# Kernel optimization log

Hardware: AMD Instinct MI355X
Metric: run time of the kernel (lower is better)

The kernel has to match this reference:

```python
import jax, jax.numpy as jnp
import numpy as np
import math

V, E, H, L, HID, T, B = 32000, 1024, 16, 4, 4096, 1024, 4
HS = E // H  # head size = 64


def _ln(x, g, b, eps=1e-5):
    m = jnp.mean(x, axis=-1, keepdims=True)
    v = jnp.var(x, axis=-1, keepdims=True)
    return (x - m) * jax.lax.rsqrt(v + eps) * g + b


def _pos_encoding(t, e):
    pos = jnp.arange(t, dtype=jnp.float32)[:, None]
    div = jnp.exp(jnp.arange(0, e, 2, dtype=jnp.float32) * (-math.log(10000.0) / e))
    pe = jnp.zeros((t, e), dtype=jnp.float32)
    pe = pe.at[:, 0::2].set(jnp.sin(pos * div))
    pe = pe.at[:, 1::2].set(jnp.cos(pos * div))
    return pe


def setup_inputs() -> dict:
    key = jax.random.key(0)
    ks = jax.random.split(key, 16)
    std = 0.02
    inp = {
        'idx': jax.random.randint(ks[0], (B, T), 0, V),
        'targets': jax.random.randint(ks[1], (B, T), 0, V),
        'tok_emb': jax.random.normal(ks[2], (V, E), jnp.float32) * std,
        'ln1_g': jnp.ones((L, E), jnp.float32),
        'ln1_b': jnp.zeros((L, E), jnp.float32),
        'wq': jax.random.normal(ks[3], (L, H, E, HS), jnp.float32) * std,
        'wk': jax.random.normal(ks[4], (L, H, E, HS), jnp.float32) * std,
        'wv': jax.random.normal(ks[5], (L, H, E, HS), jnp.float32) * std,
        'wo': jax.random.normal(ks[6], (L, H * HS, E), jnp.float32) * std,
        'bo': jnp.zeros((L, E), jnp.float32),
        'ln2_g': jnp.ones((L, E), jnp.float32),
        'ln2_b': jnp.zeros((L, E), jnp.float32),
        'w1': jax.random.normal(ks[7], (L, E, HID), jnp.float32) * std,
        'b1': jnp.zeros((L, HID), jnp.float32),
        'w2': jax.random.normal(ks[8], (L, HID, E), jnp.float32) * std,
        'b2': jnp.zeros((L, E), jnp.float32),
        'lnf_g': jnp.ones((E,), jnp.float32),
        'lnf_b': jnp.zeros((E,), jnp.float32),
        'lm_w': jax.random.normal(ks[9], (E, V), jnp.float32) * std,
        'lm_b': jnp.zeros((V,), jnp.float32),
    }
    return inp


def _forward(idx, targets, tok_emb, ln1_g, ln1_b, wq, wk, wv, wo, bo,
             ln2_g, ln2_b, w1, b1, w2, b2, lnf_g, lnf_b, lm_w, lm_b):
    b, t = idx.shape
    x = tok_emb[idx] * math.sqrt(E)              # [B,T,E], scaled embedding
    x = x + _pos_encoding(t, E)                  # sinusoidal pos enc
    causal = jnp.tril(jnp.ones((t, t), dtype=bool))
    scale = HS ** -0.5
    for l in range(L):
        h = _ln(x, ln1_g[l], ln1_b[l])
        q = jnp.einsum('bte,hek->bhtk', h, wq[l])
        k = jnp.einsum('bte,hek->bhtk', h, wk[l])
        v = jnp.einsum('bte,hek->bhtk', h, wv[l])
        scores = jnp.einsum('bhtk,bhsk->bhts', q, k) * scale
        scores = jnp.where(causal, scores, -jnp.inf)
        w = jax.nn.softmax(scores, axis=-1)
        o = jnp.einsum('bhts,bhsk->bhtk', w, v)
        o = o.transpose(0, 2, 1, 3).reshape(b, t, H * HS)  # concat heads
        x = x + o @ wo[l] + bo[l]
        h2 = _ln(x, ln2_g[l], ln2_b[l])
        x = x + jax.nn.relu(h2 @ w1[l] + b1[l]) @ w2[l] + b2[l]
    x = _ln(x, lnf_g, lnf_b)
    logits = x @ lm_w + lm_b                     # [B,T,V]
    logp = jax.nn.log_softmax(logits, axis=-1)
    loss = -jnp.mean(jnp.take_along_axis(logp, targets[..., None], axis=-1))
    return logits, loss


def reference(idx, targets, tok_emb, ln1_g, ln1_b, wq, wk, wv, wo, bo,
              ln2_g, ln2_b, w1, b1, w2, b2, lnf_g, lnf_b, lm_w, lm_b):
    return _forward(idx, targets, tok_emb, ln1_g, ln1_b, wq, wk, wv, wo, bo,
                    ln2_g, ln2_b, w1, b1, w2, b2, lnf_g, lnf_b, lm_w, lm_b)
```

## Files before the change

### kernel.cpp

```cpp
#include <hip/hip_runtime.h>
#include <hip/hip_bf16.h>
#include <math.h>

#define BB 4
#define TT 1024
#define BT 4096
#define EE 1024
#define HH 16
#define HSZ 64
#define LL 4
#define HID 4096
#define VV 32000
#define LOG2E 1.44269504f

typedef __attribute__((ext_vector_type(8))) __bf16 bf16x8;
typedef __attribute__((ext_vector_type(4))) float f32x4;

#define MFMA16(a, b, c) __builtin_amdgcn_mfma_f32_16x16x32_bf16((a), (b), (c), 0, 0, 0)

__device__ __forceinline__ int swz32(int row, int chunk) {
    return row * 32 + ((chunk ^ ((row >> 1) & 3)) << 3);
}

__device__ __forceinline__ void gload16(const __bf16* g, __bf16* l) {
    __builtin_amdgcn_global_load_lds(
        (const __attribute__((address_space(1))) unsigned int*)g,
        (__attribute__((address_space(3))) unsigned int*)l, 16, 0, 0);
}

__global__ __launch_bounds__(256) void transpose_conv(
    const float* __restrict__ in, __bf16* __restrict__ out,
    int R, int C, long ibs, int bdiv, long os1, long os2)
{
    __shared__ __bf16 tile[64][65];
    const int t = threadIdx.x;
    const int c0 = blockIdx.x * 64, r0 = blockIdx.y * 64;
    const int batch = blockIdx.z;
    const float* ib = in + (size_t)batch * ibs;
    __bf16* ob = out + (size_t)(batch / bdiv) * os1 + (size_t)(batch % bdiv) * os2;
#pragma unroll
    for (int p = 0; p < 4; ++p) {
        const int r = (t >> 4) + p * 16;
        const int c = (t & 15) * 4;
        float4 v = *(const float4*)(ib + (size_t)(r0 + r) * C + c0 + c);
        tile[c + 0][r] = (__bf16)v.x;
        tile[c + 1][r] = (__bf16)v.y;
        tile[c + 2][r] = (__bf16)v.z;
        tile[c + 3][r] = (__bf16)v.w;
    }
    __syncthreads();
#pragma unroll
    for (int p = 0; p < 2; ++p) {
        const int g = t + p * 256;
        const int co = g >> 3, ch = g & 7;
        bf16x8 vv;
#pragma unroll
        for (int j = 0; j < 8; ++j) vv[j] = tile[co][ch * 8 + j];
        *(bf16x8*)(ob + (size_t)(c0 + co) * R + r0 + ch * 8) = vv;
    }
}

__global__ __launch_bounds__(256) void embed_kernel(
    const int* __restrict__ idx, const float* __restrict__ emb, float* __restrict__ x)
{
    const int row = blockIdx.x, tid = threadIdx.x;
    const float pos = (float)(row & (TT - 1));
    const int tok = idx[row];
    const int cb = tid * 4;
    float4 ev = *(const float4*)(emb + (size_t)tok * EE + cb);
    const float kk = -9.2103403720f / (float)EE;
    float pe[4];
#pragma unroll
    for (int j = 0; j < 4; ++j) {
        const int c = cb + j;
        const float div = expf(kk * (float)(c & ~1));
        const float ang = pos * div;
        pe[j] = (c & 1) ? cosf(ang) : sinf(ang);
    }
    float4 r;
    r.x = ev.x * 32.0f + pe[0];
    r.y = ev.y * 32.0f + pe[1];
    r.z = ev.z * 32.0f + pe[2];
    r.w = ev.w * 32.0f + pe[3];
    *(float4*)(x + (size_t)row * EE + cb) = r;
}

__global__ __launch_bounds__(256) void ln_kernel(
    const float* __restrict__ x, const float* __restrict__ g,
    const float* __restrict__ be, __bf16* __restrict__ out)
{
    __shared__ float red[2][4];
    const int row = blockIdx.x, tid = threadIdx.x;
    float4 v = *(const float4*)(x + (size_t)row * EE + tid * 4);
    float s = v.x + v.y + v.z + v.w;
    float ss = v.x * v.x + v.y * v.y + v.z * v.z + v.w * v.w;
#pragma unroll
    for (int m = 1; m < 64; m <<= 1) { s += __shfl_xor(s, m); ss += __shfl_xor(ss, m); }
    if ((tid & 63) == 0) { red[0][tid >> 6] = s; red[1][tid >> 6] = ss; }
    __syncthreads();
    s  = red[0][0] + red[0][1] + red[0][2] + red[0][3];
    ss = red[1][0] + red[1][1] + red[1][2] + red[1][3];
    const float mean = s * (1.0f / EE);
    const float var  = ss * (1.0f / EE) - mean * mean;
    const float rs   = rsqrtf(var + 1e-5f);
    float4 gv = *(const float4*)(g + tid * 4);
    float4 bv = *(const float4*)(be + tid * 4);
    __bf16* o = out + (size_t)row * EE + tid * 4;
    o[0] = (__bf16)((v.x - mean) * rs * gv.x + bv.x);
    o[1] = (__bf16)((v.y - mean) * rs * gv.y + bv.y);
    o[2] = (__bf16)((v.z - mean) * rs * gv.z + bv.z);
    o[3] = (__bf16)((v.w - mean) * rs * gv.w + bv.w);
}

template <int MODE, int GSWZ, int BN>
__global__ __launch_bounds__(256, 2) void gemm_bt(
    const __bf16* __restrict__ A, const __bf16* __restrict__ Bt,
    const float* __restrict__ bias, float* __restrict__ C,
    __bf16* __restrict__ Cb, float2* __restrict__ part,
    int M, int N, int K)
{
    constexpr int JW  = BN / 32;
    constexpr int BSW = BN / 64;
    __shared__ __bf16 As[128 * 32];
    __shared__ __bf16 Bs[BN * 32];
    __shared__ float2 red[(MODE == 4) ? 128 : 1][2];

    const int tid = threadIdx.x;
    const int lane = tid & 63, wid = tid >> 6;
    const int wr = wid >> 1, wc = wid & 1;
    int bm, bn;
    if (GSWZ) {
        const int b = blockIdx.x;
        const int j = b >> 3;
        bm = (b & 7) * 4 + (j & 3);
        bn = j >> 2;
    } else {
        bm = blockIdx.y; bn = blockIdx.x;
    }
    const int m0 = bm * 128, n0 = bn * BN;

    size_t sA[2];  int loA[2];
#pragma unroll
    for (int c = 0; c < 2; ++c) {
        const int seg = wid * 2 + c;
        const int rl = seg * 16 + (lane >> 2);
        const int cl = (lane & 3) ^ ((rl >> 1) & 3);
        loA[c] = seg * 512;
        sA[c] = (size_t)(m0 + rl) * K + cl * 8;
    }
    size_t sB[BSW]; int loB[BSW];
#pragma unroll
    for (int c = 0; c < BSW; ++c) {
        const int seg = wid * BSW + c;
        const int rl = seg * 16 + (lane >> 2);
        const int cl = (lane & 3) ^ ((rl >> 1) & 3);
        loB[c] = seg * 512;
        sB[c] = (size_t)(n0 + rl) * K + cl * 8;
    }

    const int l15 = lane & 15, kch = lane >> 4;
    const int abase = swz32(wr * 64 + l15, kch);
    const int bbase = swz32(wc * (BN / 2) + l15, kch);

    f32x4 acc[4][JW] = {};

    const int nk = K >> 5;
    for (int kt = 0; kt < nk; ++kt) {
        const size_t ko = (size_t)kt * 32;
#pragma unroll
        for (int c = 0; c < 2; ++c)   gload16(A + sA[c] + ko, As + loA[c]);
#pragma unroll
        for (int c = 0; c < BSW; ++c) gload16(Bt + sB[c] + ko, Bs + loB[c]);
        __syncthreads();
        bf16x8 af[4], bfr[JW];
#pragma unroll
        for (int i = 0; i < 4; ++i)  af[i]  = *(const bf16x8*)(As + abase + i * 512);
#pragma unroll
        for (int j = 0; j < JW; ++j) bfr[j] = *(const bf16x8*)(Bs + bbase + j * 512);
#pragma unroll
        for (int i = 0; i < 4; ++i)
#pragma unroll
            for (int j = 0; j < JW; ++j)
                acc[i][j] = MFMA16(af[i], bfr[j], acc[i][j]);
        __syncthreads();
    }

    const int crow = m0 + wr * 64 + ((lane >> 4) << 2);
    const int ccol = n0 + wc * (BN / 2) + l15;
#pragma unroll
    for (int i = 0; i < 4; ++i)
#pragma unroll
        for (int j = 0; j < JW; ++j) {
            const int cc = ccol + j * 16;
#pragma unroll
            for (int r = 0; r < 4; ++r) {
                const size_t oidx = (size_t)(crow + i * 16 + r) * N + cc;
                float v = acc[i][j][r];
                if (MODE == 0) {
                    Cb[oidx] = (__bf16)v;
                } else if (MODE == 1) {
                    v += bias[cc];
                    Cb[oidx] = (__bf16)(v > 0.0f ? v : 0.0f);
                } else if (MODE == 2) {
                    C[oidx] += v + bias[cc];
                } else {
                    __builtin_nontemporal_store(v + bias[cc], &C[oidx]);
                }
            }
        }

    if constexpr (MODE == 4) {
        const int lg = lane >> 4;
#pragma unroll
        for (int i = 0; i < 4; ++i)
#pragma unroll
            for (int r = 0; r < 4; ++r) {
                float tv[4];
                float mx = -1e30f;
#pragma unroll
                for (int j = 0; j < 4; ++j) {
                    tv[j] = acc[i][j][r] + bias[ccol + j * 16];
                    mx = fmaxf(mx, tv[j]);
                }
                mx = fmaxf(mx, __shfl_xor(mx, 1));
                mx = fmaxf(mx, __shfl_xor(mx, 2));
                mx = fmaxf(mx, __shfl_xor(mx, 4));
                mx = fmaxf(mx, __shfl_xor(mx, 8));
                float sm = 0.0f;
#pragma unroll
                for (int j = 0; j < 4; ++j) sm += exp2f((tv[j] - mx) * LOG2E);
                sm += __shfl_xor(sm, 1);
                sm += __shfl_xor(sm, 2);
                sm += __shfl_xor(sm, 4);
                sm += __shfl_xor(sm, 8);
                if (l15 == 0)
                    red[wr * 64 + i * 16 + lg * 4 + r][wc] = make_float2(mx, sm);
            }
        __syncthreads();
        if (tid < 128) {
            const float2 a = red[tid][0], b = red[tid][1];
            const float M2 = fmaxf(a.x, b.x);
            const float S = a.y * exp2f((a.x - M2) * LOG2E)
                          + b.y * exp2f((b.x - M2) * LOG2E);
            part[(size_t)(m0 + tid) * (N >> 7) + bn] = make_float2(M2, S);
        }
    }
}

__global__ __launch_bounds__(64) void attn_kernel(
    const __bf16* __restrict__ qkv, __bf16* __restrict__ out)
{
    __shared__ __bf16 Pl[16 * 32];
    __shared__ __bf16 Vt[64 * 32];
    const int lane = threadIdx.x;
    const int bh = blockIdx.x, b = bh >> 4, hh = bh & 15;
    const int qbase = blockIdx.y * 16;
    const int RS = 3 * EE;
    const __bf16* qp = qkv + (size_t)(b * TT) * RS + hh * HSZ;
    const __bf16* kp = qp + EE;
    const __bf16* vp = qp + 2 * EE;
    const int l15 = lane & 15, lg = lane >> 4;

    bf16x8 aq[2];
#pragma unroll
    for (int e = 0; e < 2; ++e)
        aq[e] = *(const bf16x8*)(qp + (size_t)(qbase + l15) * RS + e * 32 + lg * 8);

    f32x4 ao[4] = {};
    float mrun[4], lrun[4];
#pragma unroll
    for (int r = 0; r < 4; ++r) { mrun[r] = -1e30f; lrun[r] = 0.0f; }

    const int ntile = qbase / 32 + 1;
    for (int st = 0; st < ntile; ++st) {
        const int sbase = st * 32;
        f32x4 as[2] = {};
        __builtin_amdgcn_s_setprio(1);
#pragma unroll
        for (int n = 0; n < 2; ++n)
#pragma unroll
            for (int e = 0; e < 2; ++e) {
                bf16x8 bk = *(const bf16x8*)(kp + (size_t)(sbase + n * 16 + l15) * RS + e * 32 + lg * 8);
                as[n] = MFMA16(aq[e], bk, as[n]);
            }
        __builtin_amdgcn_s_setprio(0);
        {
            const int sl = lane >> 1;
            const int e0 = (lane & 1) * 32;
            const __bf16* vr = vp + (size_t)(sbase + sl) * RS + e0;
#pragma unroll
            for (int c = 0; c < 4; ++c) {
                bf16x8 vvv = *(const bf16x8*)(vr + c * 8);
#pragma unroll
                for (int j = 0; j < 8; ++j)
                    Vt[swz32(e0 + c * 8 + j, sl >> 3) + (sl & 7)] = vvv[j];
            }
        }
#pragma unroll
        for (int r = 0; r < 4; ++r) {
            const int qi = qbase + lg * 4 + r;
            float sc0 = as[0][r] * 0.125f;
            float sc1 = as[1][r] * 0.125f;
            if (sbase + l15 > qi)      sc0 = -1e30f;
            if (sbase + 16 + l15 > qi) sc1 = -1e30f;
            float rm = fmaxf(sc0, sc1);
            rm = fmaxf(rm, __shfl_xor(rm, 1));
            rm = fmaxf(rm, __shfl_xor(rm, 2));
            rm = fmaxf(rm, __shfl_xor(rm, 4));
            rm = fmaxf(rm, __shfl_xor(rm, 8));
            const float mnew = fmaxf(mrun[r], rm);
            const float alpha = exp2f((mrun[r] - mnew) * LOG2E);
            const float p0 = exp2f((sc0 - mnew) * LOG2E);
            const float p1 = exp2f((sc1 - mnew) * LOG2E);
            float rs = p0 + p1;
            rs += __shfl_xor(rs, 1);
            rs += __shfl_xor(rs, 2);
            rs += __shfl_xor(rs, 4);
            rs += __shfl_xor(rs, 8);
            lrun[r] = lrun[r] * alpha + rs;
            mrun[r] = mnew;
#pragma unroll
            for (int n = 0; n < 4; ++n) ao[n][r] *= alpha;
            const int prow = lg * 4 + r;
            Pl[swz32(prow, l15 >> 3) + (l15 & 7)] = (__bf16)p0;
            Pl[swz32(prow, (16 + l15) >> 3) + (l15 & 7)] = (__bf16)p1;
        }
        asm volatile("s_waitcnt lgkmcnt(0)" ::: "memory");
        bf16x8 pa = *(const bf16x8*)(&Pl[swz32(l15, lg)]);
        __builtin_amdgcn_s_setprio(1);
#pragma unroll
        for (int n = 0; n < 4; ++n) {
            bf16x8 bv = *(const bf16x8*)(&Vt[swz32(n * 16 + l15, lg)]);
            ao[n] = MFMA16(pa, bv, ao[n]);
        }
        __builtin_amdgcn_s_setprio(0);
        asm volatile("s_waitcnt lgkmcnt(0)" ::: "memory");
    }
#pragma unroll
    for (int r = 0; r < 4; ++r) {
        const float inv = 1.0f / lrun[r];
        const int row = qbase + lg * 4 + r;
#pragma unroll
        for (int n = 0; n < 4; ++n)
            out[(size_t)(b * TT + row) * EE + hh * HSZ + n * 16 + l15] =
                (__bf16)(ao[n][r] * inv);
    }
}

__global__ __launch_bounds__(256) void loss_reduce(
    const float2* __restrict__ part, const float* __restrict__ logits,
    const int* __restrict__ tgt, float* __restrict__ lossv)
{
    __shared__ float rm[4], rs2[4];
    const int row = blockIdx.x, tid = threadIdx.x;
    float m = -1e30f, s = 0.0f;
    if (tid < (VV >> 7)) {
        const float2 p = part[(size_t)row * (VV >> 7) + tid];
        m = p.x; s = p.y;
    }
#pragma unroll
    for (int k = 1; k < 64; k <<= 1) {
        const float mo = __shfl_xor(m, k), so = __shfl_xor(s, k);
        const float mn = fmaxf(m, mo);
        s = s * exp2f((m - mn) * LOG2E) + so * exp2f((mo - mn) * LOG2E);
        m = mn;
    }
    if ((tid & 63) == 0) { rm[tid >> 6] = m; rs2[tid >> 6] = s; }
    __syncthreads();
    if (tid == 0) {
        float M = rm[0];
#pragma unroll
        for (int w = 1; w < 4; ++w) M = fmaxf(M, rm[w]);
        float S = 0.0f;
#pragma unroll
        for (int w = 0; w < 4; ++w) S += rs2[w] * exp2f((rm[w] - M) * LOG2E);
        lossv[row] = M + logf(S) - logits[(size_t)row * VV + tgt[row]];
    }
}

__global__ __launch_bounds__(256) void loss_final(const float* __restrict__ lossv, float* __restrict__ out)
{
    __shared__ float red[4];
    const int tid = threadIdx.x;
    float s = 0.0f;
    for (int i = tid; i < BT; i += 256) s += lossv[i];
#pragma unroll
    for (int k = 1; k < 64; k <<= 1) s += __shfl_xor(s, k);
    if ((tid & 63) == 0) red[tid >> 6] = s;
    __syncthreads();
    if (tid == 0) out[0] = (red[0] + red[1] + red[2] + red[3]) * (1.0f / BT);
}

extern "C" void kernel_launch(void* const* d_in, const int* in_sizes, int n_in,
                              void* d_out, int out_size, void* d_ws, size_t ws_size,
                              hipStream_t stream)
{
    const int*   idx   = (const int*)d_in[0];
    const int*   tgt   = (const int*)d_in[1];
    const float* temb  = (const float*)d_in[2];
    const float* ln1g  = (const float*)d_in[3];
    const float* ln1b  = (const float*)d_in[4];
    const float* wq    = (const float*)d_in[5];
    const float* wk    = (const float*)d_in[6];
    const float* wv    = (const float*)d_in[7];
    const float* wo    = (const float*)d_in[8];
    const float* bo    = (const float*)d_in[9];
    const float* ln2g  = (const float*)d_in[10];
    const float* ln2b  = (const float*)d_in[11];
    const float* w1    = (const float*)d_in[12];
    const float* b1    = (const float*)d_in[13];
    const float* w2    = (const float*)d_in[14];
    const float* b2    = (const float*)d_in[15];
    const float* lnfg  = (const float*)d_in[16];
    const float* lnfb  = (const float*)d_in[17];
    const float* lm_w  = (const float*)d_in[18];
    const float* lm_b  = (const float*)d_in[19];

    float* logits  = (float*)d_out;
    float* lossout = logits + (size_t)BT * VV;

    char* ws = (char*)d_ws;
    size_t off = 0;
    auto carve = [&](size_t bytes) {
        void* p = ws + off;
        off += (bytes + 255) & ~(size_t)255;
        return p;
    };
    __bf16* WQKVT = (__bf16*)carve((size_t)LL * 3072 * 1024 * 2);
    __bf16* WOT   = (__bf16*)carve((size_t)LL * 1024 * 1024 * 2);
    __bf16* W1T   = (__bf16*)carve((size_t)LL * 4096 * 1024 * 2);
    __bf16* W2T   = (__bf16*)carve((size_t)LL * 1024 * 4096 * 2);
    __bf16* LMT   = (__bf16*)carve((size_t)VV * 1024 * 2);
    float*  x     = (float*)carve((size_t)BT * EE * 4);
    __bf16* h     = (__bf16*)carve((size_t)BT * EE * 2);
    __bf16* qkv   = (__bf16*)carve((size_t)BT * 3072 * 2);
    __bf16* mid   = (__bf16*)carve((size_t)BT * HID * 2);
    float*  lossv = (float*)carve((size_t)BT * 4);
    float2* part  = (float2*)mid;

    const dim3 blk(256);

    transpose_conv<<<dim3(1, 16, 64), blk, 0, stream>>>(wq, WQKVT,           1024, 64,   65536, 16, 3145728, 65536);
    transpose_conv<<<dim3(1, 16, 64), blk, 0, stream>>>(wk, WQKVT + 1048576, 1024, 64,   65536, 16, 3145728, 65536);
    transpose_conv<<<dim3(1, 16, 64), blk, 0, stream>>>(wv, WQKVT + 2097152, 1024, 64,   65536, 16, 3145728, 65536);
    transpose_conv<<<dim3(16, 16, 4), blk, 0, stream>>>(wo, WOT,   1024, 1024, 1048576, 4, 0, 1048576);
    transpose_conv<<<dim3(64, 16, 4), blk, 0, stream>>>(w1, W1T,   1024, 4096, 4194304, 4, 0, 4194304);
    transpose_conv<<<dim3(16, 64, 4), blk, 0, stream>>>(w2, W2T,   4096, 1024, 4194304, 4, 0, 4194304);
    transpose_conv<<<dim3(500, 16, 1), blk, 0, stream>>>(lm_w, LMT, 1024, 32000, 0, 1, 0, 0);

    embed_kernel<<<BT, blk, 0, stream>>>(idx, temb, x);

    for (int l = 0; l < LL; ++l) {
        ln_kernel<<<BT, blk, 0, stream>>>(x, ln1g + l * EE, ln1b + l * EE, h);
        gemm_bt<0, 0, 128><<<dim3(24, 32), blk, 0, stream>>>(h, WQKVT + (size_t)l * 3145728,
                                                             nullptr, nullptr, qkv, nullptr, BT, 3072, 1024);
        attn_kernel<<<dim3(64, 64), dim3(64), 0, stream>>>(qkv, h);
        gemm_bt<2, 0, 64><<<dim3(16, 32), blk, 0, stream>>>(h, WOT + (size_t)l * 1048576,
                                                            bo + l * EE, x, nullptr, nullptr, BT, 1024, 1024);
        ln_kernel<<<BT, blk, 0, stream>>>(x, ln2g + l * EE, ln2b + l * EE, h);
        gemm_bt<1, 0, 128><<<dim3(32, 32), blk, 0, stream>>>(h, W1T + (size_t)l * 4194304,
                                                             b1 + l * HID, nullptr, mid, nullptr, BT, 4096, 1024);
        gemm_bt<2, 0, 64><<<dim3(16, 32), blk, 0, stream>>>(mid, W2T + (size_t)l * 4194304,
                                                            b2 + l * EE, x, nullptr, nullptr, BT, 1024, 4096);
    }
    ln_kernel<<<BT, blk, 0, stream>>>(x, lnfg, lnfb, h);
    gemm_bt<4, 1, 128><<<dim3(8000), blk, 0, stream>>>(h, LMT, lm_b, logits, nullptr, part, BT, VV, 1024);
    loss_reduce<<<BT, blk, 0, stream>>>(part, logits, tgt, lossv);
    loss_final<<<1, blk, 0, stream>>>(lossv, lossout);
}
```

Measured before the change: 1.644 ms.

## Add 256x256 double-buffered 8-wave GEMM for QKV, FFN1 and LM head

Adds a new GEMM kernel with 256x256 output tiles, 512 threads and a double-buffered LDS pipeline. Async global-to-LDS loads for the next k-step are interleaved with MFMA phases. The QKV, FFN-up and LM-head GEMMs (with its fused softmax partials) now use it, with grid swizzling and partials resized to V/256 per row. The aim is more data reuse per loaded byte and better latency hiding. In exchange it uses much more LDS and more registers, and the LM head drops its nontemporal store.

```diff
diff --git a/kernel.cpp b/kernel.cpp
--- a/kernel.cpp
+++ b/kernel.cpp
@@ -27,6 +27,8 @@
         (const __attribute__((address_space(1))) unsigned int*)g,
         (__attribute__((address_space(3))) unsigned int*)l, 16, 0, 0);
 }
+
+#define BAR() do { asm volatile("" ::: "memory"); __builtin_amdgcn_s_barrier(); asm volatile("" ::: "memory"); } while (0)
 
 __global__ __launch_bounds__(256) void transpose_conv(
     const float* __restrict__ in, __bf16* __restrict__ out,
@@ -112,32 +114,180 @@
     o[3] = (__bf16)((v.w - mean) * rs * gv.w + bv.w);
 }
 
-template <int MODE, int GSWZ, int BN>
-__global__ __launch_bounds__(256, 2) void gemm_bt(
+template <int MODE>
+__global__ __launch_bounds__(512, 2) void gemm256(
     const __bf16* __restrict__ A, const __bf16* __restrict__ Bt,
     const float* __restrict__ bias, float* __restrict__ C,
     __bf16* __restrict__ Cb, float2* __restrict__ part,
     int M, int N, int K)
 {
+    __shared__ __bf16 As[2][2][256 * 32];
+    __shared__ __bf16 Bs[2][2][256 * 32];
+    __shared__ float2 lred[(MODE == 4) ? 256 : 1][(MODE == 4) ? 4 : 1];
+
+    const int tid = threadIdx.x;
+    const int lane = tid & 63, wid = tid >> 6;
+    const int wm = wid >> 2, wn = wid & 3;
+    const int nwg = gridDim.x;
+    const int b = blockIdx.x;
+    const int gj = (b & 7) * (nwg >> 3) + (b >> 3);
+    const int bm = gj & 15, bn = gj >> 4;
+    const int m0 = bm * 256, n0 = bn * 256;
+    const int l15 = lane & 15, lg = lane >> 4;
+
+    const int rl = (wid << 4) + (lane >> 2);
+    const int cl = (lane & 3) ^ ((rl >> 1) & 3);
+    const int ldso = (wid << 4) * 32;
+    const size_t ga = (size_t)(m0 + rl) * K + cl * 8;
+    const size_t gb = (size_t)(n0 + rl) * K + cl * 8;
+    const size_t rowhK = (size_t)128 * K;
+
+    auto stageA = [&](int buf, int kh, int kt) {
+        const size_t go = (size_t)kt * 64 + (size_t)kh * 32;
+        gload16(A + ga + go,         &As[buf][kh][ldso]);
+        gload16(A + ga + rowhK + go, &As[buf][kh][4096 + ldso]);
+    };
+    auto stageB = [&](int buf, int kh, int kt) {
+        const size_t go = (size_t)kt * 64 + (size_t)kh * 32;
+        gload16(Bt + gb + go,         &Bs[buf][kh][ldso]);
+        gload16(Bt + gb + rowhK + go, &Bs[buf][kh][4096 + ldso]);
+    };
+
+    f32x4 acc[8][4] = {};
+
+    auto ldA = [&](bf16x8 (&af)[4], int cur, int kh, int qi) {
+#pragma unroll
+        for (int i = 0; i < 4; ++i)
+            af[i] = *(const bf16x8*)(&As[cur][kh][swz32(wm * 128 + (qi * 4 + i) * 16 + l15, lg)]);
+    };
+    auto ldB = [&](bf16x8 (&bf)[4], int cur, int kh) {
+#pragma unroll
+        for (int j = 0; j < 4; ++j)
+            bf[j] = *(const bf16x8*)(&Bs[cur][kh][swz32(wn * 64 + j * 16 + l15, lg)]);
+    };
+    auto mm = [&](bf16x8 (&af)[4], bf16x8 (&bf)[4], int qi) {
+        __builtin_amdgcn_s_setprio(1);
+#pragma unroll
+        for (int i = 0; i < 4; ++i)
+#pragma unroll
+            for (int j = 0; j < 4; ++j)
+                acc[qi * 4 + i][j] = MFMA16(af[i], bf[j], acc[qi * 4 + i][j]);
+        __builtin_amdgcn_s_setprio(0);
+    };
+
+    const int nkt = K >> 6;
+
+    stageB(0, 0, 0); stageA(0, 0, 0); stageB(0, 1, 0); stageA(0, 1, 0);
+    stageB(1, 0, 1); stageA(1, 0, 1); stageB(1, 1, 1);
+    asm volatile("s_waitcnt vmcnt(10)" ::: "memory");
+    BAR();
+
+    for (int g = 0; g < nkt; ++g) {
+        const int cur = g & 1;
+        const int kA1 = (g + 1 < nkt) ? g + 1 : nkt - 1;
+        const int kN  = (g + 2 < nkt) ? g + 2 : nkt - 1;
+        bf16x8 af[4], bf[4];
+        ldA(af, cur, 0, 0); ldB(bf, cur, 0);
+        stageA(cur ^ 1, 1, kA1);
+        BAR();
+        mm(af, bf, 0);
+        BAR();
+        ldA(af, cur, 0, 1);
+        stageB(cur, 0, kN);
+        asm volatile("s_waitcnt vmcnt(10)" ::: "memory");
+        BAR();
+        mm(af, bf, 1);
+        BAR();
+        ldA(af, cur, 1, 0); ldB(bf, cur, 1);
+        stageA(cur, 0, kN);
+        BAR();
+        mm(af, bf, 0);
+        BAR();
+        ldA(af, cur, 1, 1);
+        stageB(cur, 1, kN);
+        asm volatile("s_waitcnt vmcnt(10)" ::: "memory");
+        BAR();
+        mm(af, bf, 1);
+        BAR();
+    }
+    asm volatile("s_waitcnt vmcnt(0)" ::: "memory");
+
+    const int crow = m0 + wm * 128;
+    const int ccol = n0 + wn * 64 + l15;
+#pragma unroll
+    for (int fi = 0; fi < 8; ++fi)
+#pragma unroll
+        for (int j = 0; j < 4; ++j) {
+            const int cc = ccol + j * 16;
+#pragma unroll
+            for (int r = 0; r < 4; ++r) {
+                const size_t oidx = (size_t)(crow + fi * 16 + lg * 4 + r) * N + cc;
+                float v = acc[fi][j][r];
+                if (MODE == 0) {
+                    Cb[oidx] = (__bf16)v;
+                } else if (MODE == 1) {
+                    v += bias[cc];
+                    Cb[oidx] = (__bf16)(v > 0.0f ? v : 0.0f);
+                } else {
+                    C[oidx] = v + bias[cc];
+                }
+            }
+        }
+
+    if constexpr (MODE == 4) {
+#pragma unroll
+        for (int fi = 0; fi < 8; ++fi)
+#pragma unroll
+            for (int r = 0; r < 4; ++r) {
+                float tv[4];
+                float mx = -1e30f;
+#pragma unroll
+                for (int j = 0; j < 4; ++j) {
+                    tv[j] = acc[fi][j][r] + bias[ccol + j * 16];
+                    mx = fmaxf(mx, tv[j]);
+                }
+                mx = fmaxf(mx, __shfl_xor(mx, 1));
+                mx = fmaxf(mx, __shfl_xor(mx, 2));
+                mx = fmaxf(mx, __shfl_xor(mx, 4));
+                mx = fmaxf(mx, __shfl_xor(mx, 8));
+                float sm = 0.0f;
+#pragma unroll
+                for (int j = 0; j < 4; ++j) sm += exp2f((tv[j] - mx) * LOG2E);
+                sm += __shfl_xor(sm, 1);
+                sm += __shfl_xor(sm, 2);
+                sm += __shfl_xor(sm, 4);
+                sm += __shfl_xor(sm, 8);
+                if (l15 == 0)
+                    lred[wm * 128 + fi * 16 + lg * 4 + r][wn] = make_float2(mx, sm);
+            }
+        BAR();
+        if (tid < 256) {
+            float M2 = -1e30f;
+#pragma unroll
+            for (int w = 0; w < 4; ++w) M2 = fmaxf(M2, lred[tid][w].x);
+            float S = 0.0f;
+#pragma unroll
+            for (int w = 0; w < 4; ++w) S += lred[tid][w].y * exp2f((lred[tid][w].x - M2) * LOG2E);
+            part[(size_t)(m0 + tid) * (N >> 8) + bn] = make_float2(M2, S);
+        }
+    }
+}
+
+template <int MODE, int BN>
+__global__ __launch_bounds__(256, 2) void gemm_bt(
+    const __bf16* __restrict__ A, const __bf16* __restrict__ Bt,
+    const float* __restrict__ bias, float* __restrict__ C,
+    __bf16* __restrict__ Cb, int M, int N, int K)
+{
     constexpr int JW  = BN / 32;
     constexpr int BSW = BN / 64;
     __shared__ __bf16 As[128 * 32];
     __shared__ __bf16 Bs[BN * 32];
-    __shared__ float2 red[(MODE == 4) ? 128 : 1][2];
 
     const int tid = threadIdx.x;
     const int lane = tid & 63, wid = tid >> 6;
     const int wr = wid >> 1, wc = wid & 1;
-    int bm, bn;
-    if (GSWZ) {
-        const int b = blockIdx.x;
-        const int j = b >> 3;
-        bm = (b & 7) * 4 + (j & 3);
-        bn = j >> 2;
-    } else {
-        bm = blockIdx.y; bn = blockIdx.x;
-    }
-    const int m0 = bm * 128, n0 = bn * BN;
+    const int m0 = blockIdx.y * 128, n0 = blockIdx.x * BN;
 
     size_t sA[2];  int loA[2];
 #pragma unroll
@@ -204,47 +354,10 @@
                 } else if (MODE == 2) {
                     C[oidx] += v + bias[cc];
                 } else {
-                    __builtin_nontemporal_store(v + bias[cc], &C[oidx]);
+                    C[oidx] = v + bias[cc];
                 }
             }
         }
-
-    if constexpr (MODE == 4) {
-        const int lg = lane >> 4;
-#pragma unroll
-        for (int i = 0; i < 4; ++i)
-#pragma unroll
-            for (int r = 0; r < 4; ++r) {
-                float tv[4];
-                float mx = -1e30f;
-#pragma unroll
-                for (int j = 0; j < 4; ++j) {
-                    tv[j] = acc[i][j][r] + bias[ccol + j * 16];
-                    mx = fmaxf(mx, tv[j]);
-                }
-                mx = fmaxf(mx, __shfl_xor(mx, 1));
-                mx = fmaxf(mx, __shfl_xor(mx, 2));
-                mx = fmaxf(mx, __shfl_xor(mx, 4));
-                mx = fmaxf(mx, __shfl_xor(mx, 8));
-                float sm = 0.0f;
-#pragma unroll
-                for (int j = 0; j < 4; ++j) sm += exp2f((tv[j] - mx) * LOG2E);
-                sm += __shfl_xor(sm, 1);
-                sm += __shfl_xor(sm, 2);
-                sm += __shfl_xor(sm, 4);
-                sm += __shfl_xor(sm, 8);
-                if (l15 == 0)
-                    red[wr * 64 + i * 16 + lg * 4 + r][wc] = make_float2(mx, sm);
-            }
-        __syncthreads();
-        if (tid < 128) {
-            const float2 a = red[tid][0], b = red[tid][1];
-            const float M2 = fmaxf(a.x, b.x);
-            const float S = a.y * exp2f((a.x - M2) * LOG2E)
-                          + b.y * exp2f((b.x - M2) * LOG2E);
-            part[(size_t)(m0 + tid) * (N >> 7) + bn] = make_float2(M2, S);
-        }
-    }
 }
 
 __global__ __launch_bounds__(64) void attn_kernel(
@@ -349,13 +462,13 @@
 
 __global__ __launch_bounds__(256) void loss_reduce(
     const float2* __restrict__ part, const float* __restrict__ logits,
-    const int* __restrict__ tgt, float* __restrict__ lossv)
+    const int* __restrict__ tgt, float* __restrict__ lossv, int NP)
 {
     __shared__ float rm[4], rs2[4];
     const int row = blockIdx.x, tid = threadIdx.x;
     float m = -1e30f, s = 0.0f;
-    if (tid < (VV >> 7)) {
-        const float2 p = part[(size_t)row * (VV >> 7) + tid];
+    if (tid < NP) {
+        const float2 p = part[(size_t)row * NP + tid];
         m = p.x; s = p.y;
     }
 #pragma unroll
@@ -452,19 +565,19 @@
 
     for (int l = 0; l < LL; ++l) {
         ln_kernel<<<BT, blk, 0, stream>>>(x, ln1g + l * EE, ln1b + l * EE, h);
-        gemm_bt<0, 0, 128><<<dim3(24, 32), blk, 0, stream>>>(h, WQKVT + (size_t)l * 3145728,
-                                                             nullptr, nullptr, qkv, nullptr, BT, 3072, 1024);
+        gemm256<0><<<dim3(192), dim3(512), 0, stream>>>(h, WQKVT + (size_t)l * 3145728,
+                                                        nullptr, nullptr, qkv, nullptr, BT, 3072, 1024);
         attn_kernel<<<dim3(64, 64), dim3(64), 0, stream>>>(qkv, h);
-        gemm_bt<2, 0, 64><<<dim3(16, 32), blk, 0, stream>>>(h, WOT + (size_t)l * 1048576,
-                                                            bo + l * EE, x, nullptr, nullptr, BT, 1024, 1024);
+        gemm_bt<2, 64><<<dim3(16, 32), blk, 0, stream>>>(h, WOT + (size_t)l * 1048576,
+                                                         bo + l * EE, x, nullptr, BT, 1024, 1024);
         ln_kernel<<<BT, blk, 0, stream>>>(x, ln2g + l * EE, ln2b + l * EE, h);
-        gemm_bt<1, 0, 128><<<dim3(32, 32), blk, 0, stream>>>(h, W1T + (size_t)l * 4194304,
-                                                             b1 + l * HID, nullptr, mid, nullptr, BT, 4096, 1024);
-        gemm_bt<2, 0, 64><<<dim3(16, 32), blk, 0, stream>>>(mid, W2T + (size_t)l * 4194304,
-                                                            b2 + l * EE, x, nullptr, nullptr, BT, 1024, 4096);
+        gemm256<1><<<dim3(256), dim3(512), 0, stream>>>(h, W1T + (size_t)l * 4194304,
+                                                        b1 + l * HID, nullptr, mid, nullptr, BT, 4096, 1024);
+        gemm_bt<2, 64><<<dim3(16, 32), blk, 0, stream>>>(mid, W2T + (size_t)l * 4194304,
+                                                         b2 + l * EE, x, nullptr, BT, 1024, 4096);
     }
     ln_kernel<<<BT, blk, 0, stream>>>(x, lnfg, lnfb, h);
-    gemm_bt<4, 1, 128><<<dim3(8000), blk, 0, stream>>>(h, LMT, lm_b, logits, nullptr, part, BT, VV, 1024);
-    loss_reduce<<<BT, blk, 0, stream>>>(part, logits, tgt, lossv);
+    gemm256<4><<<dim3(2000), dim3(512), 0, stream>>>(h, LMT, lm_b, logits, nullptr, part, BT, VV, 1024);
+    loss_reduce<<<BT, blk, 0, stream>>>(part, logits, tgt, lossv, VV >> 8);
     loss_final<<<1, blk, 0, stream>>>(lossv, lossout);
 }
```

Result: slower. 1.808 ms (+10.0%).

## Widen attention key tiles to 64, mask only the last tile, reorder grid

Applied to the files above, without the earlier changes.

The attention kernel now handles 64 keys per loop step instead of 32. This halves the number of online-softmax rescale steps and shuffle reductions, and gives two MFMAs per output fragment for the PV product, with a new 64-wide swizzled LDS layout for P and the transposed V. The causal mask is applied only on the final key tile. The grid axes are swapped so that consecutive blocks share the same batch-head, which should improve L2 reuse of K and V. The logits store in the LM-head GEMM changes from a nontemporal store to a plain store, and loss_reduce takes the partial count as a parameter. The trade-off is more LDS use and register pressure per block in attention, plus a different cache policy for the large logits write.

```diff
diff --git a/kernel.cpp b/kernel.cpp
--- a/kernel.cpp
+++ b/kernel.cpp
@@ -20,6 +20,10 @@
 
 __device__ __forceinline__ int swz32(int row, int chunk) {
     return row * 32 + ((chunk ^ ((row >> 1) & 3)) << 3);
+}
+
+__device__ __forceinline__ int swz64(int row, int chunk) {
+    return row * 64 + ((chunk ^ (row & 7)) << 3);
 }
 
 __device__ __forceinline__ void gload16(const __bf16* g, __bf16* l) {
@@ -204,7 +208,7 @@
                 } else if (MODE == 2) {
                     C[oidx] += v + bias[cc];
                 } else {
-                    __builtin_nontemporal_store(v + bias[cc], &C[oidx]);
+                    C[oidx] = v + bias[cc];
                 }
             }
         }
@@ -250,11 +254,11 @@
 __global__ __launch_bounds__(64) void attn_kernel(
     const __bf16* __restrict__ qkv, __bf16* __restrict__ out)
 {
-    __shared__ __bf16 Pl[16 * 32];
-    __shared__ __bf16 Vt[64 * 32];
+    __shared__ __bf16 Pl[16 * 64];
+    __shared__ __bf16 Vt[64 * 64];
     const int lane = threadIdx.x;
-    const int bh = blockIdx.x, b = bh >> 4, hh = bh & 15;
-    const int qbase = blockIdx.y * 16;
+    const int bh = blockIdx.y, b = bh >> 4, hh = bh & 15;
+    const int qbase = blockIdx.x * 16;
     const int RS = 3 * EE;
     const __bf16* qp = qkv + (size_t)(b * TT) * RS + hh * HSZ;
     const __bf16* kp = qp + EE;
@@ -271,13 +275,13 @@
 #pragma unroll
     for (int r = 0; r < 4; ++r) { mrun[r] = -1e30f; lrun[r] = 0.0f; }
 
-    const int ntile = qbase / 32 + 1;
+    const int ntile = (qbase >> 6) + 1;
     for (int st = 0; st < ntile; ++st) {
-        const int sbase = st * 32;
-        f32x4 as[2] = {};
+        const int sbase = st * 64;
+        f32x4 as[4] = {};
         __builtin_amdgcn_s_setprio(1);
 #pragma unroll
-        for (int n = 0; n < 2; ++n)
+        for (int n = 0; n < 4; ++n)
 #pragma unroll
             for (int e = 0; e < 2; ++e) {
                 bf16x8 bk = *(const bf16x8*)(kp + (size_t)(sbase + n * 16 + l15) * RS + e * 32 + lg * 8);
@@ -285,34 +289,40 @@
             }
         __builtin_amdgcn_s_setprio(0);
         {
-            const int sl = lane >> 1;
-            const int e0 = (lane & 1) * 32;
-            const __bf16* vr = vp + (size_t)(sbase + sl) * RS + e0;
-#pragma unroll
-            for (int c = 0; c < 4; ++c) {
-                bf16x8 vvv = *(const bf16x8*)(vr + c * 8);
-#pragma unroll
-                for (int j = 0; j < 8; ++j)
-                    Vt[swz32(e0 + c * 8 + j, sl >> 3) + (sl & 7)] = vvv[j];
+            const __bf16* vr = vp + (size_t)(sbase + lane) * RS;
+            const int kc = lane >> 3, kw = lane & 7;
+#pragma unroll
+            for (int c = 0; c < 8; ++c) {
+                bf16x8 vv = *(const bf16x8*)(vr + c * 8);
+#pragma unroll
+                for (int j = 0; j < 8; ++j) {
+                    const int e = c * 8 + j;
+                    Vt[e * 64 + ((kc ^ (e & 7)) << 3) + kw] = vv[j];
+                }
             }
         }
+        const bool lastt = (st == ntile - 1);
 #pragma unroll
         for (int r = 0; r < 4; ++r) {
             const int qi = qbase + lg * 4 + r;
-            float sc0 = as[0][r] * 0.125f;
-            float sc1 = as[1][r] * 0.125f;
-            if (sbase + l15 > qi)      sc0 = -1e30f;
-            if (sbase + 16 + l15 > qi) sc1 = -1e30f;
-            float rm = fmaxf(sc0, sc1);
+            float sc[4];
+#pragma unroll
+            for (int n = 0; n < 4; ++n) sc[n] = as[n][r] * 0.125f;
+            if (lastt) {
+#pragma unroll
+                for (int n = 0; n < 4; ++n)
+                    if (sbase + n * 16 + l15 > qi) sc[n] = -1e30f;
+            }
+            float rm = fmaxf(fmaxf(sc[0], sc[1]), fmaxf(sc[2], sc[3]));
             rm = fmaxf(rm, __shfl_xor(rm, 1));
             rm = fmaxf(rm, __shfl_xor(rm, 2));
             rm = fmaxf(rm, __shfl_xor(rm, 4));
             rm = fmaxf(rm, __shfl_xor(rm, 8));
             const float mnew = fmaxf(mrun[r], rm);
             const float alpha = exp2f((mrun[r] - mnew) * LOG2E);
-            const float p0 = exp2f((sc0 - mnew) * LOG2E);
-            const float p1 = exp2f((sc1 - mnew) * LOG2E);
-            float rs = p0 + p1;
+            float p[4], rs = 0.0f;
+#pragma unroll
+            for (int n = 0; n < 4; ++n) { p[n] = exp2f((sc[n] - mnew) * LOG2E); rs += p[n]; }
             rs += __shfl_xor(rs, 1);
             rs += __shfl_xor(rs, 2);
             rs += __shfl_xor(rs, 4);
@@ -322,17 +332,25 @@
 #pragma unroll
             for (int n = 0; n < 4; ++n) ao[n][r] *= alpha;
             const int prow = lg * 4 + r;
-            Pl[swz32(prow, l15 >> 3) + (l15 & 7)] = (__bf16)p0;
-            Pl[swz32(prow, (16 + l15) >> 3) + (l15 & 7)] = (__bf16)p1;
+#pragma unroll
+            for (int n = 0; n < 4; ++n) {
+                const int key = n * 16 + l15;
+                Pl[prow * 64 + (((key >> 3) ^ (prow & 7)) << 3) + (key & 7)] = (__bf16)p[n];
+            }
         }
         asm volatile("s_waitcnt lgkmcnt(0)" ::: "memory");
-        bf16x8 pa = *(const bf16x8*)(&Pl[swz32(l15, lg)]);
+        bf16x8 pa[2];
+#pragma unroll
+        for (int kf = 0; kf < 2; ++kf)
+            pa[kf] = *(const bf16x8*)(&Pl[swz64(l15, kf * 4 + lg)]);
         __builtin_amdgcn_s_setprio(1);
 #pragma unroll
-        for (int n = 0; n < 4; ++n) {
-            bf16x8 bv = *(const bf16x8*)(&Vt[swz32(n * 16 + l15, lg)]);
-            ao[n] = MFMA16(pa, bv, ao[n]);
-        }
+        for (int n = 0; n < 4; ++n)
+#pragma unroll
+            for (int kf = 0; kf < 2; ++kf) {
+                bf16x8 bv = *(const bf16x8*)(&Vt[swz64(n * 16 + l15, kf * 4 + lg)]);
+                ao[n] = MFMA16(pa[kf], bv, ao[n]);
+            }
         __builtin_amdgcn_s_setprio(0);
         asm volatile("s_waitcnt lgkmcnt(0)" ::: "memory");
     }
@@ -349,13 +367,13 @@
 
 __global__ __launch_bounds__(256) void loss_reduce(
     const float2* __restrict__ part, const float* __restrict__ logits,
-    const int* __restrict__ tgt, float* __restrict__ lossv)
+    const int* __restrict__ tgt, float* __restrict__ lossv, int NP)
 {
     __shared__ float rm[4], rs2[4];
     const int row = blockIdx.x, tid = threadIdx.x;
     float m = -1e30f, s = 0.0f;
-    if (tid < (VV >> 7)) {
-        const float2 p = part[(size_t)row * (VV >> 7) + tid];
+    if (tid < NP) {
+        const float2 p = part[(size_t)row * NP + tid];
         m = p.x; s = p.y;
     }
 #pragma unroll
@@ -465,6 +483,6 @@
     }
     ln_kernel<<<BT, blk, 0, stream>>>(x, lnfg, lnfb, h);
     gemm_bt<4, 1, 128><<<dim3(8000), blk, 0, stream>>>(h, LMT, lm_b, logits, nullptr, part, BT, VV, 1024);
-    loss_reduce<<<BT, blk, 0, stream>>>(part, logits, tgt, lossv);
+    loss_reduce<<<BT, blk, 0, stream>>>(part, logits, tgt, lossv, VV >> 7);
     loss_final<<<1, blk, 0, stream>>>(lossv, lossout);
 }
```

Measured after the change: 2.029 ms. 23.4% more time.

## Add 256x128-tile 512-thread GEMM for QKV, FFN1 and LM head

Applied to the files above, without the earlier changes.

Adds a second GEMM kernel with 256x128 output tiles and 8 waves per block. The QKV projection, the first FFN matmul and the LM-head (with its fused softmax partials) now use it, while the residual-add GEMMs keep the old kernel. Larger tiles raise arithmetic intensity and cut redundant A/B reloads. In exchange there are fewer blocks, more LDS and register pressure, and a simpler single-buffered K loop. The LM-head output also switches from nontemporal stores to regular stores.

```diff
diff --git a/kernel.cpp b/kernel.cpp
--- a/kernel.cpp
+++ b/kernel.cpp
@@ -112,32 +112,21 @@
     o[3] = (__bf16)((v.w - mean) * rs * gv.w + bv.w);
 }
 
-template <int MODE, int GSWZ, int BN>
+template <int MODE, int BN>
 __global__ __launch_bounds__(256, 2) void gemm_bt(
     const __bf16* __restrict__ A, const __bf16* __restrict__ Bt,
     const float* __restrict__ bias, float* __restrict__ C,
-    __bf16* __restrict__ Cb, float2* __restrict__ part,
-    int M, int N, int K)
+    __bf16* __restrict__ Cb, int M, int N, int K)
 {
     constexpr int JW  = BN / 32;
     constexpr int BSW = BN / 64;
     __shared__ __bf16 As[128 * 32];
     __shared__ __bf16 Bs[BN * 32];
-    __shared__ float2 red[(MODE == 4) ? 128 : 1][2];
 
     const int tid = threadIdx.x;
     const int lane = tid & 63, wid = tid >> 6;
     const int wr = wid >> 1, wc = wid & 1;
-    int bm, bn;
-    if (GSWZ) {
-        const int b = blockIdx.x;
-        const int j = b >> 3;
-        bm = (b & 7) * 4 + (j & 3);
-        bn = j >> 2;
-    } else {
-        bm = blockIdx.y; bn = blockIdx.x;
-    }
-    const int m0 = bm * 128, n0 = bn * BN;
+    const int m0 = blockIdx.y * 128, n0 = blockIdx.x * BN;
 
     size_t sA[2];  int loA[2];
 #pragma unroll
@@ -204,13 +193,103 @@
                 } else if (MODE == 2) {
                     C[oidx] += v + bias[cc];
                 } else {
-                    __builtin_nontemporal_store(v + bias[cc], &C[oidx]);
+                    C[oidx] = v + bias[cc];
                 }
             }
         }
+}
+
+template <int MODE, int GSWZ>
+__global__ __launch_bounds__(512, 2) void gemm_bt2(
+    const __bf16* __restrict__ A, const __bf16* __restrict__ Bt,
+    const float* __restrict__ bias, float* __restrict__ C,
+    __bf16* __restrict__ Cb, float2* __restrict__ part,
+    int M, int N, int K)
+{
+    __shared__ __bf16 As[256 * 32];
+    __shared__ __bf16 Bs[128 * 32];
+    __shared__ float2 red[(MODE == 4) ? 256 : 1][2];
+
+    const int tid = threadIdx.x;
+    const int lane = tid & 63, wid = tid >> 6;
+    const int wm = wid >> 1, wn = wid & 1;
+    int bm, bn;
+    if (GSWZ) {
+        const int b = blockIdx.x;
+        const int j = b >> 3;
+        bm = (b & 7) * 2 + (j & 1);
+        bn = j >> 1;
+    } else {
+        bm = blockIdx.y; bn = blockIdx.x;
+    }
+    const int m0 = bm * 256, n0 = bn * 128;
+    const int l15 = lane & 15, lg = lane >> 4;
+
+    size_t sA[2];  int loA[2];
+#pragma unroll
+    for (int c = 0; c < 2; ++c) {
+        const int seg = wid * 2 + c;
+        const int rl = seg * 16 + (lane >> 2);
+        const int cl = (lane & 3) ^ ((rl >> 1) & 3);
+        loA[c] = seg * 512;
+        sA[c] = (size_t)(m0 + rl) * K + cl * 8;
+    }
+    size_t sB;  int loB;
+    {
+        const int rl = wid * 16 + (lane >> 2);
+        const int cl = (lane & 3) ^ ((rl >> 1) & 3);
+        loB = wid * 512;
+        sB = (size_t)(n0 + rl) * K + cl * 8;
+    }
+
+    const int abase = swz32(wm * 64 + l15, lg);
+    const int bbase = swz32(wn * 64 + l15, lg);
+
+    f32x4 acc[4][4] = {};
+
+    const int nk = K >> 5;
+    for (int kt = 0; kt < nk; ++kt) {
+        const size_t ko = (size_t)kt * 32;
+        gload16(A + sA[0] + ko, As + loA[0]);
+        gload16(A + sA[1] + ko, As + loA[1]);
+        gload16(Bt + sB + ko, Bs + loB);
+        __syncthreads();
+        bf16x8 af[4], bfr[4];
+#pragma unroll
+        for (int i = 0; i < 4; ++i) af[i]  = *(const bf16x8*)(As + abase + i * 512);
+#pragma unroll
+        for (int j = 0; j < 4; ++j) bfr[j] = *(const bf16x8*)(Bs + bbase + j * 512);
+#pragma unroll
+        for (int i = 0; i < 4; ++i)
+#pragma unroll
+            for (int j = 0; j < 4; ++j)
+                acc[i][j] = MFMA16(af[i], bfr[j], acc[i][j]);
+        __syncthreads();
+    }
+
+    const int crow = m0 + wm * 64 + lg * 4;
+    const int ccol = n0 + wn * 64 + l15;
+#pragma unroll
+    for (int i = 0; i < 4; ++i)
+#pragma unroll
+        for (int j = 0; j < 4; ++j) {
+            const int cc = ccol + j * 16;
+#pragma unroll
+            for (int r = 0; r < 4; ++r) {
+                const size_t oidx = (size_t)(crow + i * 16 + r) * N + cc;
+                float v = acc[i][j][r];
+                if (MODE == 0) {
+                    Cb[oidx] = (__bf16)v;
+                } else if (MODE == 1) {
+                    v += bias[cc];
+                    Cb[oidx] = (__bf16)(v > 0.0f ? v : 0.0f);
+                } else {
+                    C[oidx] = v + bias[cc];
+                }
+            }
+        }
 
     if constexpr (MODE == 4) {
-        const int lg = lane >> 4;
 #pragma unroll
         for (int i = 0; i < 4; ++i)
 #pragma unroll
@@ -234,14 +313,14 @@
                 sm += __shfl_xor(sm, 4);
                 sm += __shfl_xor(sm, 8);
                 if (l15 == 0)
-                    red[wr * 64 + i * 16 + lg * 4 + r][wc] = make_float2(mx, sm);
+                    red[wm * 64 + i * 16 + lg * 4 + r][wn] = make_float2(mx, sm);
             }
         __syncthreads();
-        if (tid < 128) {
-            const float2 a = red[tid][0], b = red[tid][1];
-            const float M2 = fmaxf(a.x, b.x);
+        if (tid < 256) {
+            const float2 a = red[tid][0], b2 = red[tid][1];
+            const float M2 = fmaxf(a.x, b2.x);
             const float S = a.y * exp2f((a.x - M2) * LOG2E)
-                          + b.y * exp2f((b.x - M2) * LOG2E);
+                          + b2.y * exp2f((b2.x - M2) * LOG2E);
             part[(size_t)(m0 + tid) * (N >> 7) + bn] = make_float2(M2, S);
         }
     }
@@ -349,13 +428,13 @@
 
 __global__ __launch_bounds__(256) void loss_reduce(
     const float2* __restrict__ part, const float* __restrict__ logits,
-    const int* __restrict__ tgt, float* __restrict__ lossv)
+    const int* __restrict__ tgt, float* __restrict__ lossv, int NP)
 {
     __shared__ float rm[4], rs2[4];
     const int row = blockIdx.x, tid = threadIdx.x;
     float m = -1e30f, s = 0.0f;
-    if (tid < (VV >> 7)) {
-        const float2 p = part[(size_t)row * (VV >> 7) + tid];
+    if (tid < NP) {
+        const float2 p = part[(size_t)row * NP + tid];
         m = p.x; s = p.y;
     }
 #pragma unroll
@@ -452,19 +531,19 @@
 
     for (int l = 0; l < LL; ++l) {
         ln_kernel<<<BT, blk, 0, stream>>>(x, ln1g + l * EE, ln1b + l * EE, h);
-        gemm_bt<0, 0, 128><<<dim3(24, 32), blk, 0, stream>>>(h, WQKVT + (size_t)l * 3145728,
-                                                             nullptr, nullptr, qkv, nullptr, BT, 3072, 1024);
+        gemm_bt2<0, 0><<<dim3(24, 16), dim3(512), 0, stream>>>(h, WQKVT + (size_t)l * 3145728,
+                                                               nullptr, nullptr, qkv, nullptr, BT, 3072, 1024);
         attn_kernel<<<dim3(64, 64), dim3(64), 0, stream>>>(qkv, h);
-        gemm_bt<2, 0, 64><<<dim3(16, 32), blk, 0, stream>>>(h, WOT + (size_t)l * 1048576,
-                                                            bo + l * EE, x, nullptr, nullptr, BT, 1024, 1024);
+        gemm_bt<2, 64><<<dim3(16, 32), blk, 0, stream>>>(h, WOT + (size_t)l * 1048576,
+                                                         bo + l * EE, x, nullptr, BT, 1024, 1024);
         ln_kernel<<<BT, blk, 0, stream>>>(x, ln2g + l * EE, ln2b + l * EE, h);
-        gemm_bt<1, 0, 128><<<dim3(32, 32), blk, 0, stream>>>(h, W1T + (size_t)l * 4194304,
-                                                             b1 + l * HID, nullptr, mid, nullptr, BT, 4096, 1024);
-        gemm_bt<2, 0, 64><<<dim3(16, 32), blk, 0, stream>>>(mid, W2T + (size_t)l * 4194304,
-                                                            b2 + l * EE, x, nullptr, nullptr, BT, 1024, 4096);
+        gemm_bt2<1, 0><<<dim3(32, 16), dim3(512), 0, stream>>>(h, W1T + (size_t)l * 4194304,
+                                                               b1 + l * HID, nullptr, mid, nullptr, BT, 4096, 1024);
+        gemm_bt<2, 64><<<dim3(16, 32), blk, 0, stream>>>(mid, W2T + (size_t)l * 4194304,
+                                                         b2 + l * EE, x, nullptr, BT, 1024, 4096);
     }
     ln_kernel<<<BT, blk, 0, stream>>>(x, lnfg, lnfb, h);
-    gemm_bt<4, 1, 128><<<dim3(8000), blk, 0, stream>>>(h, LMT, lm_b, logits, nullptr, part, BT, VV, 1024);
-    loss_reduce<<<BT, blk, 0, stream>>>(part, logits, tgt, lossv);
+    gemm_bt2<4, 1><<<dim3(4000), dim3(512), 0, stream>>>(h, LMT, lm_b, logits, nullptr, part, BT, VV, 1024);
+    loss_reduce<<<BT, blk, 0, stream>>>(part, logits, tgt, lossv, VV >> 7);
     loss_final<<<1, blk, 0, stream>>>(lossv, lossout);
 }
```

After: 1.674 ms. About the same (+1.8%).
